# Performance work log

Hardware: AMD Instinct MI355X
Metric: run time of the kernel (lower is better)

Reference implementation:

```python
import jax, jax.numpy as jnp
import numpy as np

NUM_HEADS = 16
NUM_KV_HEADS = 4
HEAD_DIM = 64
HIDDEN = 1024
BATCH, SEQ = 2, 2048
CAUSAL = False


def _rotate_half(x):
    x1, x2 = jnp.split(x, 2, axis=-1)
    return jnp.concatenate([-x2, x1], axis=-1)


def setup_inputs() -> dict:
    key = jax.random.key(0)
    k1, k2, k3 = jax.random.split(key, 3)
    hidden_states = jax.random.normal(k1, (BATCH, SEQ, HIDDEN), dtype=jnp.float32)
    # realistic rotary tables
    inv_freq = 1.0 / (10000.0 ** (np.arange(0, HEAD_DIM, 2, dtype=np.float32) / HEAD_DIM))
    t = np.arange(SEQ, dtype=np.float32)
    freqs = np.outer(t, inv_freq)                      # [S, D/2]
    emb = np.concatenate([freqs, freqs], axis=-1)      # [S, D]
    cos = jnp.asarray(np.cos(emb), dtype=jnp.float32)
    sin = jnp.asarray(np.sin(emb), dtype=jnp.float32)
    qkv_out = (NUM_HEADS + 2 * NUM_KV_HEADS) * HEAD_DIM
    w_qkv = jax.random.normal(k2, (qkv_out, HIDDEN), dtype=jnp.float32) * (HIDDEN ** -0.5)
    w_o = jax.random.normal(k3, (HIDDEN, NUM_HEADS * HEAD_DIM), dtype=jnp.float32) * ((NUM_HEADS * HEAD_DIM) ** -0.5)
    return {"hidden_states": hidden_states, "cos": cos, "sin": sin, "w_qkv": w_qkv, "w_o": w_o}


def reference(hidden_states, cos, sin, w_qkv, w_o):
    b, s, _ = hidden_states.shape
    qkv = jnp.einsum('bsh,oh->bso', hidden_states, w_qkv)
    qkv = qkv.reshape(b, s, NUM_HEADS + 2 * NUM_KV_HEADS, HEAD_DIM)
    q = qkv[:, :, :NUM_HEADS]                                    # [b,s,Hq,d]
    k = qkv[:, :, NUM_HEADS:NUM_HEADS + NUM_KV_HEADS]            # [b,s,Hkv,d]
    v = qkv[:, :, NUM_HEADS + NUM_KV_HEADS:]                     # [b,s,Hkv,d]
    # RoPE (HF style): broadcast cos/sin [s,d] over batch and heads
    c = cos[None, :, None, :]
    sn = sin[None, :, None, :]
    q = q * c + _rotate_half(q) * sn
    k = k * c + _rotate_half(k) * sn
    # GQA: repeat kv heads to match q heads
    rep = NUM_HEADS // NUM_KV_HEADS
    k = jnp.repeat(k, rep, axis=2)
    v = jnp.repeat(v, rep, axis=2)
    scale = HEAD_DIM ** -0.5
    scores = jnp.einsum('bqhd,bkhd->bhqk', q, k) * scale
    if CAUSAL:
        mask = jnp.tril(jnp.ones((s, s), dtype=bool))
        scores = jnp.where(mask[None, None], scores, jnp.finfo(scores.dtype).min)
    probs = jax.nn.softmax(scores, axis=-1)
    attn = jnp.einsum('bhqk,bkhd->bqhd', probs, v)
    attn = attn.reshape(b, s, NUM_HEADS * HEAD_DIM)
    return jnp.einsum('bso,ho->bsh', attn, w_o)
```

## Files before the change

kernel.cpp:

```cpp
#include <hip/hip_runtime.h>
#include <hip/hip_bf16.h>

typedef unsigned short u16;
typedef unsigned int u32;
typedef __attribute__((ext_vector_type(8))) short short8;
typedef __attribute__((ext_vector_type(4))) float f32x4;
typedef __attribute__((ext_vector_type(16))) float f32x16;
typedef __attribute__((ext_vector_type(4))) u32 u32x4;

__device__ __forceinline__ u16 f2b(float f) {
    __hip_bfloat16 h = __float2bfloat16(f);
    return *reinterpret_cast<u16*>(&h);
}
__device__ __forceinline__ float b2f(u16 u) {
    __hip_bfloat16 h;
    *reinterpret_cast<u16*>(&h) = u;
    return __bfloat162float(h);
}
__device__ __forceinline__ u32 cvtpk(float lo, float hi_) {
    u32 r;
    asm("v_cvt_pk_bf16_f32 %0, %1, %2" : "=v"(r) : "v"(lo), "v"(hi_));
    return r;
}
__device__ __forceinline__ float fexp2p(float x) {
    float nf = __builtin_rintf(x);
    float f = x - nf;
    float p = __builtin_fmaf(f, 0.05550411f, 0.24022651f);
    p = __builtin_fmaf(f, p, 0.69314718f);
    p = __builtin_fmaf(f, p, 1.0f);
    int n = (int)nf;
    float r;
    asm("v_ldexp_f32 %0, %1, %2" : "=v"(r) : "v"(p), "v"(n));
    return r;
}
__device__ __forceinline__ void gload16(const void* g, void* l) {
    __builtin_amdgcn_global_load_lds(
        (const __attribute__((address_space(1))) unsigned int*)g,
        (__attribute__((address_space(3))) unsigned int*)l, 16, 0, 0);
}

__global__ void convert_kernel(const float* __restrict__ X, const float* __restrict__ W1,
                               const float* __restrict__ W2,
                               u16* __restrict__ Xb, u16* __restrict__ W1b, u16* __restrict__ W2b) {
    int idx = blockIdx.x * 256 + threadIdx.x;
    const float* src; u16* dst; int off;
    if (idx < 1048576)        { src = X;  dst = Xb;  off = idx; }
    else if (idx < 1441792)   { src = W1; dst = W1b; off = idx - 1048576; }
    else                      { src = W2; dst = W2b; off = idx - 1441792; }
    float4 v = reinterpret_cast<const float4*>(src)[off];
    ushort4 o;
    o.x = f2b(v.x); o.y = f2b(v.y); o.z = f2b(v.z); o.w = f2b(v.w);
    reinterpret_cast<ushort4*>(dst)[off] = o;
}

template <typename OUT>
__global__ __launch_bounds__(256) void gemm_bt(const u16* __restrict__ A, const u16* __restrict__ B,
                                               OUT* __restrict__ C, int M, int N, int K) {
    __shared__ u16 As[2][64 * 64];
    __shared__ u16 Bs[2][128 * 64];
    const int tid = threadIdx.x;
    const int lane = tid & 63, wave = tid >> 6;
    const int wm = wave >> 1, wn = wave & 1;
    const int row16 = lane & 15, kgrp = lane >> 4;
    const int bm = blockIdx.x, bn = blockIdx.y;
    const int nk = K >> 6;
    const u16* Abase = A + (size_t)bm * 64 * K;
    const u16* Bbase = B + (size_t)bn * 128 * K;

    f32x4 acc[2][4];
#pragma unroll
    for (int i = 0; i < 2; ++i)
#pragma unroll
        for (int j = 0; j < 4; ++j) acc[i][j] = {0.f, 0.f, 0.f, 0.f};

    auto stage = [&](int buf, int kt) {
#pragma unroll
        for (int it = 0; it < 2; ++it) {
            int chunk = it * 256 + tid;
            int row = chunk >> 3, c = chunk & 7;
            int cs = c ^ (row & 7);
            gload16(Abase + (size_t)row * K + kt * 64 + cs * 8, &As[buf][chunk * 8]);
        }
#pragma unroll
        for (int it = 0; it < 4; ++it) {
            int chunk = it * 256 + tid;
            int row = chunk >> 3, c = chunk & 7;
            int cs = c ^ (row & 7);
            gload16(Bbase + (size_t)row * K + kt * 64 + cs * 8, &Bs[buf][chunk * 8]);
        }
    };

    stage(0, 0);
    __syncthreads();
    for (int kt = 0; kt < nk; ++kt) {
        int cur = kt & 1;
        if (kt + 1 < nk) stage(cur ^ 1, kt + 1);
        short8 af[2][2], bfr[4][2];
#pragma unroll
        for (int mf = 0; mf < 2; ++mf) {
            int r = wm * 32 + mf * 16 + row16;
#pragma unroll
            for (int kk = 0; kk < 2; ++kk)
                af[mf][kk] = *(const short8*)&As[cur][(r * 8 + ((kk * 4 + kgrp) ^ (r & 7))) * 8];
        }
#pragma unroll
        for (int nf = 0; nf < 4; ++nf) {
            int r = wn * 64 + nf * 16 + row16;
#pragma unroll
            for (int kk = 0; kk < 2; ++kk)
                bfr[nf][kk] = *(const short8*)&Bs[cur][(r * 8 + ((kk * 4 + kgrp) ^ (r & 7))) * 8];
        }
        __builtin_amdgcn_s_setprio(1);
#pragma unroll
        for (int kk = 0; kk < 2; ++kk)
#pragma unroll
            for (int mf = 0; mf < 2; ++mf)
#pragma unroll
                for (int nf = 0; nf < 4; ++nf)
                    acc[mf][nf] = __builtin_amdgcn_mfma_f32_16x16x32_bf16(af[mf][kk], bfr[nf][kk], acc[mf][nf], 0, 0, 0);
        __builtin_amdgcn_s_setprio(0);
        __syncthreads();
    }
#pragma unroll
    for (int mf = 0; mf < 2; ++mf)
#pragma unroll
        for (int r = 0; r < 4; ++r) {
            int row = bm * 64 + wm * 32 + mf * 16 + kgrp * 4 + r;
#pragma unroll
            for (int nf = 0; nf < 4; ++nf) {
                int col = bn * 128 + wn * 64 + nf * 16 + row16;
                float v = acc[mf][nf][r];
                if constexpr (sizeof(OUT) == 2) C[(size_t)row * N + col] = f2b(v);
                else                            C[(size_t)row * N + col] = v;
            }
        }
}

__global__ void rope_kernel(const u16* __restrict__ qkv, const float* __restrict__ cosb,
                            const float* __restrict__ sinb, u16* __restrict__ Qa,
                            u16* __restrict__ Ka) {
    int idx = blockIdx.x * 256 + threadIdx.x;
    if (idx < 2097152) {
        int d = idx & 31, h = (idx >> 5) & 15, m = idx >> 9;
        int s = m & 2047, b = m >> 11;
        const u16* src = qkv + (size_t)m * 1536 + h * 64 + d;
        float q1 = b2f(src[0]), q2 = b2f(src[32]);
        float c = cosb[s * 64 + d], sn = sinb[s * 64 + d];
        u16* dst = Qa + ((size_t)(b * 16 + h) * 2048 + s) * 64 + d;
        dst[0]  = f2b((q1 * c - q2 * sn) * 0.18033688f);
        dst[32] = f2b((q2 * c + q1 * sn) * 0.18033688f);
    } else {
        int t = idx - 2097152;
        int d = t & 31, kh = (t >> 5) & 3, m = t >> 7;
        int s = m & 2047, b = m >> 11;
        const u16* src = qkv + (size_t)m * 1536 + (16 + kh) * 64 + d;
        float q1 = b2f(src[0]), q2 = b2f(src[32]);
        float c = cosb[s * 64 + d], sn = sinb[s * 64 + d];
        u16* dst = Ka + ((size_t)(b * 4 + kh) * 2048 + s) * 64 + d;
        dst[0]  = f2b(q1 * c - q2 * sn);
        dst[32] = f2b(q2 * c + q1 * sn);
    }
}

__global__ __launch_bounds__(256) void vtrans_kernel(const u16* __restrict__ qkv, u16* __restrict__ Vt) {
    __shared__ u16 T[64 * 71];
    const int tid = threadIdx.x;
    const int sblk = blockIdx.x, kh = blockIdx.y, b = blockIdx.z;
    const u16* src = qkv + (size_t)(b * 2048 + sblk * 64) * 1536 + 1280 + kh * 64;
#pragma unroll
    for (int it = 0; it < 2; ++it) {
        int u = it * 256 + tid;
        int s = u >> 3, c = u & 7;
        short8 v = *(const short8*)(src + (size_t)s * 1536 + c * 8);
#pragma unroll
        for (int i = 0; i < 8; ++i)
            T[(c * 8 + i) * 71 + s] = (u16)v[i];
    }
    __syncthreads();
    u16* dst = Vt + (size_t)(b * 4 + kh) * 64 * 2048 + sblk * 64;
#pragma unroll
    for (int it = 0; it < 2; ++it) {
        int u = it * 256 + tid;
        int d = u >> 3, s0 = (u & 7) * 8;
        short8 o;
#pragma unroll
        for (int i = 0; i < 8; ++i) o[i] = (short)T[d * 71 + s0 + i];
        *(short8*)(dst + (size_t)d * 2048 + s0) = o;
    }
}

__global__ __launch_bounds__(256) void attn_kernel(const u16* __restrict__ Qa,
                                                   const u16* __restrict__ Ka,
                                                   const u16* __restrict__ Vt,
                                                   u16* __restrict__ Ob) {
    __shared__ u16 Ks[2][64 * 64];
    __shared__ u16 Vs[2][64 * 64];
    const int tid = threadIdx.x, lane = tid & 63, wave = tid >> 6;
    const int q32 = lane & 31, hi = lane >> 5;
    const int qt = blockIdx.x, h = blockIdx.y, b = blockIdx.z;
    const int kh = h >> 2;
    const u16* Qp = Qa + ((size_t)(b * 16 + h) * 2048 + qt * 128 + wave * 32) * 64;
    const u16* Kp = Ka + (size_t)(b * 4 + kh) * 2048 * 64;
    const u16* Vp = Vt + (size_t)(b * 4 + kh) * 64 * 2048;

    short8 qf[4];
#pragma unroll
    for (int dt = 0; dt < 4; ++dt)
        qf[dt] = *(const short8*)(Qp + q32 * 64 + dt * 16 + hi * 8);

    f32x16 oacc[2];
#pragma unroll
    for (int i = 0; i < 2; ++i)
#pragma unroll
        for (int r = 0; r < 16; ++r) oacc[i][r] = 0.f;
    float lpx = 0.f, lpy = 0.f;

    auto stageKV = [&](int buf, int kvt) {
#pragma unroll
        for (int it = 0; it < 2; ++it) {
            int chunk = it * 256 + tid;
            int row = chunk >> 3, c = chunk & 7;
            gload16(Kp + (size_t)(kvt * 64 + row) * 64 + ((c ^ (row & 7)) * 8), &Ks[buf][chunk * 8]);
        }
#pragma unroll
        for (int it = 0; it < 2; ++it) {
            int chunk = it * 256 + tid;
            int row = chunk >> 3, c = chunk & 7;
            gload16(Vp + (size_t)row * 2048 + kvt * 64 + ((c ^ (row & 7)) * 8), &Vs[buf][chunk * 8]);
        }
    };

    stageKV(0, 0);
    __syncthreads();
    for (int kvt = 0; kvt < 32; ++kvt) {
        const int cur = kvt & 1;
        if (kvt + 1 < 32) stageKV(cur ^ 1, kvt + 1);

        f32x16 S[2];
#pragma unroll
        for (int j = 0; j < 2; ++j)
#pragma unroll
            for (int r = 0; r < 16; ++r) S[j][r] = 0.f;
        __builtin_amdgcn_s_setprio(1);
#pragma unroll
        for (int kt2 = 0; kt2 < 2; ++kt2) {
            int krow = kt2 * 32 + q32;
#pragma unroll
            for (int dt = 0; dt < 4; ++dt) {
                short8 kf = *(const short8*)&Ks[cur][(krow * 8 + ((dt * 2 + hi) ^ (krow & 7))) * 8];
                S[kt2] = __builtin_amdgcn_mfma_f32_32x32x16_bf16(kf, qf[dt], S[kt2], 0, 0, 0);
            }
        }
        __builtin_amdgcn_s_setprio(0);

#pragma unroll
        for (int kt2 = 0; kt2 < 2; ++kt2)
#pragma unroll
            for (int r = 0; r < 16; r += 2) {
                float p0 = fexp2p(S[kt2][r]);
                float p1 = fexp2p(S[kt2][r + 1]);
                S[kt2][r] = p0; S[kt2][r + 1] = p1;
                lpx += p0; lpy += p1;
            }

        __builtin_amdgcn_s_setprio(1);
#pragma unroll
        for (int kc = 0; kc < 4; ++kc) {
            const int kt2 = kc >> 1, R = (kc & 1) * 8;
            u32 a0 = cvtpk(S[kt2][R + 0], S[kt2][R + 1]);
            u32 b0 = cvtpk(S[kt2][R + 4], S[kt2][R + 5]);
            asm("v_permlane32_swap_b32 %0, %1" : "+v"(a0), "+v"(b0));
            u32 a1 = cvtpk(S[kt2][R + 2], S[kt2][R + 3]);
            u32 b1 = cvtpk(S[kt2][R + 6], S[kt2][R + 7]);
            asm("v_permlane32_swap_b32 %0, %1" : "+v"(a1), "+v"(b1));
            u32x4 pw; pw[0] = a0; pw[1] = a1; pw[2] = b0; pw[3] = b1;
            short8 pf = __builtin_bit_cast(short8, pw);
#pragma unroll
            for (int dt2 = 0; dt2 < 2; ++dt2) {
                int vrow = dt2 * 32 + q32;
                short8 vf = *(const short8*)&Vs[cur][(vrow * 8 + ((kc * 2 + hi) ^ (vrow & 7))) * 8];
                oacc[dt2] = __builtin_amdgcn_mfma_f32_32x32x16_bf16(vf, pf, oacc[dt2], 0, 0, 0);
            }
        }
        __builtin_amdgcn_s_setprio(0);
        __syncthreads();
    }

    float lpart = lpx + lpy;
    float l = lpart + __shfl_xor(lpart, 32);
    float inv = 1.f / l;
    const size_t mbase = ((size_t)(b * 2048 + qt * 128 + wave * 32 + q32)) * 1024 + h * 64;
#pragma unroll
    for (int dt2 = 0; dt2 < 2; ++dt2)
#pragma unroll
        for (int rq = 0; rq < 4; ++rq) {
            ushort4 o;
            o.x = f2b(oacc[dt2][rq * 4 + 0] * inv);
            o.y = f2b(oacc[dt2][rq * 4 + 1] * inv);
            o.z = f2b(oacc[dt2][rq * 4 + 2] * inv);
            o.w = f2b(oacc[dt2][rq * 4 + 3] * inv);
            *(ushort4*)&Ob[mbase + dt2 * 32 + rq * 8 + hi * 4] = o;
        }
}

extern "C" void kernel_launch(void* const* d_in, const int* in_sizes, int n_in,
                              void* d_out, int out_size, void* d_ws, size_t ws_size,
                              hipStream_t stream) {
    const float* X    = (const float*)d_in[0];
    const float* cosb = (const float*)d_in[1];
    const float* sinb = (const float*)d_in[2];
    const float* Wqkv = (const float*)d_in[3];
    const float* Wo   = (const float*)d_in[4];
    float* out = (float*)d_out;
    char* ws = (char*)d_ws;

    u16* Xbf    = (u16*)(ws);
    u16* Wqkvbf = (u16*)(ws + 8388608);
    u16* Wobf   = (u16*)(ws + 11534336);
    u16* QKV    = (u16*)(ws + 13631488);
    u16* Qa     = (u16*)(ws + 26214400);
    u16* Ka     = (u16*)(ws + 34603008);
    u16* Vt     = (u16*)(ws + 36700160);
    u16* attnb  = Xbf;

    convert_kernel<<<6656, 256, 0, stream>>>(X, Wqkv, Wo, Xbf, Wqkvbf, Wobf);
    gemm_bt<u16><<<dim3(64, 12), 256, 0, stream>>>(Xbf, Wqkvbf, QKV, 4096, 1536, 1024);
    rope_kernel<<<10240, 256, 0, stream>>>(QKV, cosb, sinb, Qa, Ka);
    vtrans_kernel<<<dim3(32, 4, 2), 256, 0, stream>>>(QKV, Vt);
    attn_kernel<<<dim3(16, 16, 2), 256, 0, stream>>>(Qa, Ka, Vt, attnb);
    gemm_bt<float><<<dim3(64, 8), 256, 0, stream>>>(attnb, Wobf, out, 4096, 1024, 1024);
}
```

Baseline: 176.3 us.

## Use hardware exp2, precompute staging addresses, and set occupancy launch bounds

Replaces the polynomial exp2 approximation in attention with the hardware v_exp_f32 instruction, which uses one transcendental op instead of several FMAs plus ldexp. Staging loops in both the GEMM and attention kernels now use pointers and LDS destinations computed once and advanced by a fixed stride, instead of recomputing swizzled addresses every tile. Launch bounds add minimum-occupancy hints (3 blocks for GEMM, 2 for attention), which may cap registers and cause spills.

```diff
diff --git a/kernel.cpp b/kernel.cpp
--- a/kernel.cpp
+++ b/kernel.cpp
@@ -22,15 +22,9 @@
     asm("v_cvt_pk_bf16_f32 %0, %1, %2" : "=v"(r) : "v"(lo), "v"(hi_));
     return r;
 }
-__device__ __forceinline__ float fexp2p(float x) {
-    float nf = __builtin_rintf(x);
-    float f = x - nf;
-    float p = __builtin_fmaf(f, 0.05550411f, 0.24022651f);
-    p = __builtin_fmaf(f, p, 0.69314718f);
-    p = __builtin_fmaf(f, p, 1.0f);
-    int n = (int)nf;
+__device__ __forceinline__ float fexp2(float x) {
     float r;
-    asm("v_ldexp_f32 %0, %1, %2" : "=v"(r) : "v"(p), "v"(n));
+    asm("v_exp_f32 %0, %1" : "=v"(r) : "v"(x));
     return r;
 }
 __device__ __forceinline__ void gload16(const void* g, void* l) {
@@ -54,8 +48,8 @@
 }
 
 template <typename OUT>
-__global__ __launch_bounds__(256) void gemm_bt(const u16* __restrict__ A, const u16* __restrict__ B,
-                                               OUT* __restrict__ C, int M, int N, int K) {
+__global__ __launch_bounds__(256, 3) void gemm_bt(const u16* __restrict__ A, const u16* __restrict__ B,
+                                                  OUT* __restrict__ C, int M, int N, int K) {
     __shared__ u16 As[2][64 * 64];
     __shared__ u16 Bs[2][128 * 64];
     const int tid = threadIdx.x;
@@ -64,8 +58,17 @@
     const int row16 = lane & 15, kgrp = lane >> 4;
     const int bm = blockIdx.x, bn = blockIdx.y;
     const int nk = K >> 6;
-    const u16* Abase = A + (size_t)bm * 64 * K;
-    const u16* Bbase = B + (size_t)bn * 128 * K;
+
+    const int r0 = tid >> 3, c0s = ((tid & 7) ^ (r0 & 7)) * 8;
+    const u16* aSrc = A + (size_t)(bm * 64 + r0) * K + c0s;
+    const u16* bSrc = B + (size_t)(bn * 128 + r0) * K + c0s;
+    u16* const ad0 = &As[0][tid * 8];
+    u16* const ad1 = &As[0][(tid + 256) * 8];
+    u16* const bd0 = &Bs[0][tid * 8];
+    u16* const bd1 = &Bs[0][(tid + 256) * 8];
+    u16* const bd2 = &Bs[0][(tid + 512) * 8];
+    u16* const bd3 = &Bs[0][(tid + 768) * 8];
+    const size_t aK32 = (size_t)32 * K;
 
     f32x4 acc[2][4];
 #pragma unroll
@@ -73,28 +76,23 @@
 #pragma unroll
         for (int j = 0; j < 4; ++j) acc[i][j] = {0.f, 0.f, 0.f, 0.f};
 
-    auto stage = [&](int buf, int kt) {
-#pragma unroll
-        for (int it = 0; it < 2; ++it) {
-            int chunk = it * 256 + tid;
-            int row = chunk >> 3, c = chunk & 7;
-            int cs = c ^ (row & 7);
-            gload16(Abase + (size_t)row * K + kt * 64 + cs * 8, &As[buf][chunk * 8]);
-        }
-#pragma unroll
-        for (int it = 0; it < 4; ++it) {
-            int chunk = it * 256 + tid;
-            int row = chunk >> 3, c = chunk & 7;
-            int cs = c ^ (row & 7);
-            gload16(Bbase + (size_t)row * K + kt * 64 + cs * 8, &Bs[buf][chunk * 8]);
-        }
+    auto stage = [&](int buf) {
+        int lo = buf * 4096;
+        int lob = buf * 8192;
+        gload16(aSrc, ad0 + lo);
+        gload16(aSrc + aK32, ad1 + lo);
+        gload16(bSrc, bd0 + lob);
+        gload16(bSrc + aK32, bd1 + lob);
+        gload16(bSrc + 2 * aK32, bd2 + lob);
+        gload16(bSrc + 3 * aK32, bd3 + lob);
+        aSrc += 64; bSrc += 64;
     };
 
-    stage(0, 0);
+    stage(0);
     __syncthreads();
     for (int kt = 0; kt < nk; ++kt) {
         int cur = kt & 1;
-        if (kt + 1 < nk) stage(cur ^ 1, kt + 1);
+        if (kt + 1 < nk) stage(cur ^ 1);
         short8 af[2][2], bfr[4][2];
 #pragma unroll
         for (int mf = 0; mf < 2; ++mf) {
@@ -189,10 +187,10 @@
     }
 }
 
-__global__ __launch_bounds__(256) void attn_kernel(const u16* __restrict__ Qa,
-                                                   const u16* __restrict__ Ka,
-                                                   const u16* __restrict__ Vt,
-                                                   u16* __restrict__ Ob) {
+__global__ __launch_bounds__(256, 2) void attn_kernel(const u16* __restrict__ Qa,
+                                                      const u16* __restrict__ Ka,
+                                                      const u16* __restrict__ Vt,
+                                                      u16* __restrict__ Ob) {
     __shared__ u16 Ks[2][64 * 64];
     __shared__ u16 Vs[2][64 * 64];
     const int tid = threadIdx.x, lane = tid & 63, wave = tid >> 6;
@@ -200,8 +198,14 @@
     const int qt = blockIdx.x, h = blockIdx.y, b = blockIdx.z;
     const int kh = h >> 2;
     const u16* Qp = Qa + ((size_t)(b * 16 + h) * 2048 + qt * 128 + wave * 32) * 64;
-    const u16* Kp = Ka + (size_t)(b * 4 + kh) * 2048 * 64;
-    const u16* Vp = Vt + (size_t)(b * 4 + kh) * 64 * 2048;
+
+    const int r0 = tid >> 3, c0s = ((tid & 7) ^ (r0 & 7)) * 8;
+    const u16* kSrc = Ka + (size_t)(b * 4 + kh) * 2048 * 64 + (size_t)r0 * 64 + c0s;
+    const u16* vSrc = Vt + (size_t)(b * 4 + kh) * 64 * 2048 + (size_t)r0 * 2048 + c0s;
+    u16* const kd0 = &Ks[0][tid * 8];
+    u16* const kd1 = &Ks[0][(tid + 256) * 8];
+    u16* const vd0 = &Vs[0][tid * 8];
+    u16* const vd1 = &Vs[0][(tid + 256) * 8];
 
     short8 qf[4];
 #pragma unroll
@@ -215,26 +219,20 @@
         for (int r = 0; r < 16; ++r) oacc[i][r] = 0.f;
     float lpx = 0.f, lpy = 0.f;
 
-    auto stageKV = [&](int buf, int kvt) {
-#pragma unroll
-        for (int it = 0; it < 2; ++it) {
-            int chunk = it * 256 + tid;
-            int row = chunk >> 3, c = chunk & 7;
-            gload16(Kp + (size_t)(kvt * 64 + row) * 64 + ((c ^ (row & 7)) * 8), &Ks[buf][chunk * 8]);
-        }
-#pragma unroll
-        for (int it = 0; it < 2; ++it) {
-            int chunk = it * 256 + tid;
-            int row = chunk >> 3, c = chunk & 7;
-            gload16(Vp + (size_t)row * 2048 + kvt * 64 + ((c ^ (row & 7)) * 8), &Vs[buf][chunk * 8]);
-        }
+    auto stageKV = [&](int buf) {
+        int lo = buf * 4096;
+        gload16(kSrc,           kd0 + lo);
+        gload16(kSrc + 32 * 64, kd1 + lo);
+        gload16(vSrc,             vd0 + lo);
+        gload16(vSrc + 32 * 2048, vd1 + lo);
+        kSrc += 4096; vSrc += 64;
     };
 
-    stageKV(0, 0);
+    stageKV(0);
     __syncthreads();
     for (int kvt = 0; kvt < 32; ++kvt) {
         const int cur = kvt & 1;
-        if (kvt + 1 < 32) stageKV(cur ^ 1, kvt + 1);
+        if (kvt + 1 < 32) stageKV(cur ^ 1);
 
         f32x16 S[2];
 #pragma unroll
@@ -257,8 +255,8 @@
         for (int kt2 = 0; kt2 < 2; ++kt2)
 #pragma unroll
             for (int r = 0; r < 16; r += 2) {
-                float p0 = fexp2p(S[kt2][r]);
-                float p1 = fexp2p(S[kt2][r + 1]);
+                float p0 = fexp2(S[kt2][r]);
+                float p1 = fexp2(S[kt2][r + 1]);
                 S[kt2][r] = p0; S[kt2][r + 1] = p1;
                 lpx += p0; lpy += p1;
             }
```

Result: faster. 166.6 us (-5.5%).
